# Performance work log

Measured on AMD Instinct MI355X. Metric: run time of the kernel, lower is better.

The kernel has to match this reference:

```python
import jax, jax.numpy as jnp
import numpy as np

NHEAD = 12
EPS = 1e-5


def layernorm_nobias(x, gamma):
    mu = jnp.mean(x, axis=-1, keepdims=True)
    var = jnp.var(x, axis=-1, keepdims=True)
    return (x - mu) * jax.lax.rsqrt(var + EPS) * gamma


def setup_inputs() -> dict:
    key = jax.random.key(0)
    ks = jax.random.split(key, 10)
    b, l, d = 4, 2048, 768
    s = d ** -0.5
    return {
        "x": jax.random.normal(ks[0], (b, l, d), jnp.float32),
        "Wq": jax.random.normal(ks[1], (d, d), jnp.float32) * s,
        "Wk": jax.random.normal(ks[2], (d, d), jnp.float32) * s,
        "bk": jax.random.normal(ks[3], (d,), jnp.float32) * 0.02,
        "Wv": jax.random.normal(ks[4], (d, d), jnp.float32) * s,
        "bv": jax.random.normal(ks[5], (d,), jnp.float32) * 0.02,
        "gq": jnp.ones((d,), jnp.float32),
        "gk": jnp.ones((d,), jnp.float32),
        "Wo": jax.random.normal(ks[6], (d, d), jnp.float32) * s,
        "bo": jnp.zeros((d,), jnp.float32),
    }


def reference(x, Wq, Wk, bk, Wv, bv, gq, gk, Wo, bo):
    b, l, d = x.shape
    n = NHEAD
    hd = d // n
    scale = hd ** -0.5
    # projections (torch Linear: x @ W.T + b), QK-norm over full dmodel
    q = layernorm_nobias(x @ Wq.T, gq)
    k = layernorm_nobias(x @ Wk.T + bk, gk)
    v = x @ Wv.T + bv
    # split heads: b l (n hd) -> b n l hd
    q = q.reshape(b, l, n, hd).transpose(0, 2, 1, 3)
    k = k.reshape(b, l, n, hd).transpose(0, 2, 1, 3)
    v = v.reshape(b, l, n, hd).transpose(0, 2, 1, 3)
    # scores [b, n, l_q, l_k]; NOTE: softmax over the QUERY axis (dim=-2)
    scores = jnp.einsum('bnqd,bnkd->bnqk', q, k) * scale
    attn = jax.nn.softmax(scores, axis=-2)
    o = jnp.einsum('bnqk,bnkd->bnqd', attn, v)
    o = o.transpose(0, 2, 1, 3).reshape(b, l, d)
    return o @ Wo.T + bo + x
```

## Files before the change

### kernel.cpp

```cpp
#include <hip/hip_runtime.h>
#include <cstddef>
#include <cstdint>


typedef unsigned short u16;
typedef short  bf16x8 __attribute__((ext_vector_type(8)));
typedef float  f32x4  __attribute__((ext_vector_type(4)));
typedef unsigned short u16x8 __attribute__((ext_vector_type(8)));
typedef unsigned short u16x4 __attribute__((ext_vector_type(4)));

#define B_   4
#define L_   2048
#define D_   768
#define NH_  12
#define HD_  64
#define M_   (B_*L_)
#define SC2  (0.125f * 1.44269504088896f)

__device__ __forceinline__ float ex2(float x) { return __builtin_amdgcn_exp2f(x); }

__device__ __forceinline__ u16 f2bf(float f) {
    union { float f; unsigned u; } v; v.f = f;
    unsigned r = v.u + 0x7FFFu + ((v.u >> 16) & 1u);
    return (u16)(r >> 16);
}
__device__ __forceinline__ float bf2f(u16 b) {
    union { unsigned u; float f; } v; v.u = ((unsigned)b) << 16;
    return v.f;
}
__device__ __forceinline__ unsigned fbits(float f) {
    union { float f; unsigned u; } v; v.f = f; return v.u;
}
__device__ __forceinline__ unsigned packbf(float lo, float hi) {
    return __builtin_amdgcn_perm(fbits(hi), fbits(lo), 0x07060302u);
}

__device__ __forceinline__ void gld16(const void* g, void* l) {
    __builtin_amdgcn_global_load_lds(
        (const __attribute__((address_space(1))) unsigned*)g,
        (__attribute__((address_space(3))) unsigned*)l, 16, 0, 0);
}

__global__ __launch_bounds__(256) void cvt_all(
    const float* __restrict__ X,
    const float* __restrict__ W0, const float* __restrict__ W1,
    const float* __restrict__ W2, const float* __restrict__ W3,
    u16* __restrict__ Yx,
    u16* __restrict__ Y0, u16* __restrict__ Y1,
    u16* __restrict__ Y2, u16* __restrict__ Y3)
{
    const int nX8 = (M_ * D_) / 8;
    const int nW8 = (D_ * D_) / 8;
    int i = blockIdx.x * 256 + threadIdx.x;
    if (i >= nX8 + 4 * nW8) return;
    const float* S; u16* Dst; int off;
    if (i < nX8) { S = X; Dst = Yx; off = i; }
    else {
        int j = i - nX8;
        int w = j / nW8; off = j - w * nW8;
        S   = (w == 0) ? W0 : (w == 1) ? W1 : (w == 2) ? W2 : W3;
        Dst = (w == 0) ? Y0 : (w == 1) ? Y1 : (w == 2) ? Y2 : Y3;
    }
    const float4* xp = (const float4*)S + (size_t)off * 2;
    float4 a = xp[0], b = xp[1];
    u16x8 o;
    o[0] = f2bf(a.x); o[1] = f2bf(a.y); o[2] = f2bf(a.z); o[3] = f2bf(a.w);
    o[4] = f2bf(b.x); o[5] = f2bf(b.y); o[6] = f2bf(b.z); o[7] = f2bf(b.w);
    *((u16x8*)Dst + off) = o;
}

__global__ __launch_bounds__(256, 4) void gemm_qkv(
    const u16* __restrict__ A,
    const u16* __restrict__ W0, const u16* __restrict__ W1,
    const u16* __restrict__ W2,
    const float* __restrict__ bk, const float* __restrict__ bv,
    u16* __restrict__ q_o, u16* __restrict__ k_o, u16* __restrict__ v_o)
{
    __shared__ __align__(16) u16 lds[16384];
    __shared__ float bs[128];
    const int tid  = threadIdx.x;
    const int lane = tid & 63, w = tid >> 6;
    const int s    = lane & 15, quad = lane >> 4;
    const int bid  = blockIdx.x;
    const int xcd  = bid & 7, j0 = bid >> 3;
    const int bm   = (xcd * 8 + j0 / 18) * 128;
    const int sub  = j0 % 18;
    const int seg  = sub / 6;
    const int bn   = (sub % 6) * 128;
    const u16* W = (seg == 0) ? W0 : ((seg == 1) ? W1 : W2);
    u16* OUT = (seg == 0) ? q_o : ((seg == 1) ? k_o : v_o);
    const int mh = (w >> 1) * 64, nh = (w & 1) * 64;
    const int wb = tid & ~63;
    const int cq = quad ^ ((s >> 1) & 3);

    if (tid < 128)
        bs[tid] = (seg == 1) ? bk[bn + tid] : ((seg == 2) ? bv[bn + tid] : 0.0f);

    f32x4 acc[4][4];
    #pragma unroll
    for (int j = 0; j < 4; ++j)
        #pragma unroll
        for (int i = 0; i < 4; ++i) acc[j][i] = (f32x4){0.f, 0.f, 0.f, 0.f};

    {
        int c = tid, r = c >> 2, cs = (c & 3) ^ ((r >> 1) & 3);
        gld16(A + (size_t)(bm + r) * D_ + cs * 8, lds + (size_t)wb * 8);
        gld16(W + (size_t)(bn + r) * D_ + cs * 8, lds + 8192 + (size_t)wb * 8);
        c = tid + 256; r = c >> 2; cs = (c & 3) ^ ((r >> 1) & 3);
        gld16(A + (size_t)(bm + r) * D_ + cs * 8, lds + (size_t)(wb + 256) * 8);
        gld16(W + (size_t)(bn + r) * D_ + cs * 8, lds + 8192 + (size_t)(wb + 256) * 8);
    }
    __syncthreads();

    for (int t = 0; t < 24; ++t) {
        const u16* Ab = lds + (t & 1) * 4096;
        const u16* Bb = lds + 8192 + (t & 1) * 4096;
        if (t < 23) {
            const int k0 = (t + 1) * 32;
            u16* Ad = lds + ((t + 1) & 1) * 4096;
            u16* Bd = lds + 8192 + ((t + 1) & 1) * 4096;
            int c = tid, r = c >> 2, cs = (c & 3) ^ ((r >> 1) & 3);
            gld16(A + (size_t)(bm + r) * D_ + k0 + cs * 8, Ad + (size_t)wb * 8);
            gld16(W + (size_t)(bn + r) * D_ + k0 + cs * 8, Bd + (size_t)wb * 8);
            c = tid + 256; r = c >> 2; cs = (c & 3) ^ ((r >> 1) & 3);
            gld16(A + (size_t)(bm + r) * D_ + k0 + cs * 8, Ad + (size_t)(wb + 256) * 8);
            gld16(W + (size_t)(bn + r) * D_ + k0 + cs * 8, Bd + (size_t)(wb + 256) * 8);
        }
        bf16x8 af[4], bf[4];
        #pragma unroll
        for (int i = 0; i < 4; ++i)
            af[i] = *(const bf16x8*)(Ab + (mh + i * 16 + s) * 32 + cq * 8);
        #pragma unroll
        for (int j = 0; j < 4; ++j)
            bf[j] = *(const bf16x8*)(Bb + (nh + j * 16 + s) * 32 + cq * 8);
        #pragma unroll
        for (int j = 0; j < 4; ++j)
            #pragma unroll
            for (int i = 0; i < 4; ++i)
                acc[j][i] = __builtin_amdgcn_mfma_f32_16x16x32_bf16(
                    bf[j], af[i], acc[j][i], 0, 0, 0);
        __syncthreads();
    }
    u16* Ct = lds;
    #pragma unroll
    for (int j = 0; j < 4; ++j) {
        const int n0 = nh + j * 16 + quad * 4;
        const f32x4 b4 = *(const f32x4*)(bs + n0);
        const int cn = n0 >> 3, off = n0 & 7;
        #pragma unroll
        for (int i = 0; i < 4; ++i) {
            const int m = mh + i * 16 + s;
            u16x4 ov;
            #pragma unroll
            for (int r = 0; r < 4; ++r) ov[r] = f2bf(acc[j][i][r] + b4[r]);
            *(u16x4*)(Ct + m * 128 + ((cn ^ (m & 15)) * 8) + off) = ov;
        }
    }
    __syncthreads();
    {
        const int m = tid >> 1, half = tid & 1;
        u16* dst = OUT + (size_t)(bm + m) * D_ + bn + half * 64;
        #pragma unroll
        for (int cc = 0; cc < 8; ++cc) {
            const int cn = half * 8 + cc;
            u16x8 v = *(const u16x8*)(Ct + m * 128 + ((cn ^ (m & 15)) * 8));
            *(u16x8*)(dst + cc * 8) = v;
        }
    }
}

__global__ __launch_bounds__(256, 3) void gemm_final(
    const u16* __restrict__ A, const u16* __restrict__ W,
    const float* __restrict__ bias, const float* __restrict__ resid,
    float* __restrict__ outf)
{
    __shared__ __align__(16) u16 lds[16384];
    const int tid  = threadIdx.x;
    const int lane = tid & 63, w = tid >> 6;
    const int s    = lane & 15, quad = lane >> 4;
    const int bid  = blockIdx.x;
    const int xcd  = bid & 7, j0 = bid >> 3;
    const int bm   = (xcd * 8 + j0 / 6) * 128;
    const int bn   = (j0 % 6) * 128;
    const int mh   = (w >> 1) * 64, nh = (w & 1) * 64;
    const int wb   = tid & ~63;
    const int cq   = quad ^ ((s >> 1) & 3);
    f32x4 acc[4][4];
    #pragma unroll
    for (int j = 0; j < 4; ++j)
        #pragma unroll
        for (int i = 0; i < 4; ++i) acc[j][i] = (f32x4){0.f, 0.f, 0.f, 0.f};

    {
        int c = tid, r = c >> 2, cs = (c & 3) ^ ((r >> 1) & 3);
        gld16(A + (size_t)(bm + r) * D_ + cs * 8, lds + (size_t)wb * 8);
        gld16(W + (size_t)(bn + r) * D_ + cs * 8, lds + 8192 + (size_t)wb * 8);
        c = tid + 256; r = c >> 2; cs = (c & 3) ^ ((r >> 1) & 3);
        gld16(A + (size_t)(bm + r) * D_ + cs * 8, lds + (size_t)(wb + 256) * 8);
        gld16(W + (size_t)(bn + r) * D_ + cs * 8, lds + 8192 + (size_t)(wb + 256) * 8);
    }
    __syncthreads();

    for (int t = 0; t < 24; ++t) {
        const u16* Ab = lds + (t & 1) * 4096;
        const u16* Bb = lds + 8192 + (t & 1) * 4096;
        if (t < 23) {
            const int k0 = (t + 1) * 32;
            u16* Ad = lds + ((t + 1) & 1) * 4096;
            u16* Bd = lds + 8192 + ((t + 1) & 1) * 4096;
            int c = tid, r = c >> 2, cs = (c & 3) ^ ((r >> 1) & 3);
            gld16(A + (size_t)(bm + r) * D_ + k0 + cs * 8, Ad + (size_t)wb * 8);
            gld16(W + (size_t)(bn + r) * D_ + k0 + cs * 8, Bd + (size_t)wb * 8);
            c = tid + 256; r = c >> 2; cs = (c & 3) ^ ((r >> 1) & 3);
            gld16(A + (size_t)(bm + r) * D_ + k0 + cs * 8, Ad + (size_t)(wb + 256) * 8);
            gld16(W + (size_t)(bn + r) * D_ + k0 + cs * 8, Bd + (size_t)(wb + 256) * 8);
        }
        bf16x8 af[4], bf[4];
        #pragma unroll
        for (int i = 0; i < 4; ++i)
            af[i] = *(const bf16x8*)(Ab + (mh + i * 16 + s) * 32 + cq * 8);
        #pragma unroll
        for (int j = 0; j < 4; ++j)
            bf[j] = *(const bf16x8*)(Bb + (nh + j * 16 + s) * 32 + cq * 8);
        #pragma unroll
        for (int j = 0; j < 4; ++j)
            #pragma unroll
            for (int i = 0; i < 4; ++i)
                acc[j][i] = __builtin_amdgcn_mfma_f32_16x16x32_bf16(
                    bf[j], af[i], acc[j][i], 0, 0, 0);
        __syncthreads();
    }
    #pragma unroll
    for (int j = 0; j < 4; ++j) {
        const int n0 = nh + j * 16 + quad * 4;
        const float4 b4 = *(const float4*)(bias + bn + n0);
        #pragma unroll
        for (int i = 0; i < 4; ++i) {
            const int m = mh + i * 16 + s;
            const size_t base = (size_t)(bm + m) * D_ + bn + n0;
            const float4 rs = *(const float4*)(resid + base);
            float4 o;
            o.x = acc[j][i][0] + b4.x + rs.x;
            o.y = acc[j][i][1] + b4.y + rs.y;
            o.z = acc[j][i][2] + b4.z + rs.z;
            o.w = acc[j][i][3] + b4.w + rs.w;
            *(float4*)(outf + base) = o;
        }
    }
}

__global__ __launch_bounds__(256) void ln2_bf16(
    const u16* __restrict__ Q, const u16* __restrict__ K,
    const float* __restrict__ gq, const float* __restrict__ gk,
    u16* __restrict__ Yq, u16* __restrict__ Yk)
{
    const int which = blockIdx.y;
    const int rowi  = threadIdx.x >> 5;
    const int l32   = threadIdx.x & 31;
    const int row   = blockIdx.x * 8 + rowi;
    const u16* x = (which ? K : Q) + (size_t)row * D_ + l32 * 24;
    const float* gamma = (which ? gk : gq) + l32 * 24;
    u16* Y = (which ? Yk : Yq) + (size_t)row * D_ + l32 * 24;
    const float scale = which ? 1.0f : (float)SC2;

    u16x8 vv[3];
    float f[24];
    float lsum = 0.f, lsq = 0.f;
    #pragma unroll
    for (int e = 0; e < 3; ++e) {
        vv[e] = *(const u16x8*)(x + e * 8);
        #pragma unroll
        for (int k = 0; k < 8; ++k) {
            float t = bf2f(vv[e][k]);
            f[e * 8 + k] = t; lsum += t; lsq += t * t;
        }
    }
    #pragma unroll
    for (int off = 16; off > 0; off >>= 1) {
        lsum += __shfl_xor(lsum, off);
        lsq  += __shfl_xor(lsq,  off);
    }
    const float mu  = lsum * (1.0f / D_);
    const float var = lsq * (1.0f / D_) - mu * mu;
    const float inv = rsqrtf(var + 1e-5f) * scale;
    #pragma unroll
    for (int e = 0; e < 3; ++e) {
        const float4 ga = *(const float4*)(gamma + e * 8);
        const float4 gb = *(const float4*)(gamma + e * 8 + 4);
        u16x8 o;
        o[0] = f2bf((f[e*8+0] - mu) * inv * ga.x);
        o[1] = f2bf((f[e*8+1] - mu) * inv * ga.y);
        o[2] = f2bf((f[e*8+2] - mu) * inv * ga.z);
        o[3] = f2bf((f[e*8+3] - mu) * inv * ga.w);
        o[4] = f2bf((f[e*8+4] - mu) * inv * gb.x);
        o[5] = f2bf((f[e*8+5] - mu) * inv * gb.y);
        o[6] = f2bf((f[e*8+6] - mu) * inv * gb.z);
        o[7] = f2bf((f[e*8+7] - mu) * inv * gb.w);
        *(u16x8*)(Y + e * 8) = o;
    }
}

__global__ __launch_bounds__(256, 3) void attn_stats(
    const u16* __restrict__ Qb, const u16* __restrict__ Kb,
    const u16* __restrict__ Vb, u16* __restrict__ Vt)
{
    __shared__ __align__(16) u16 Ks[128 * 64];
    __shared__ __align__(16) u16 Qs[2][128 * 64];
    __shared__ float lbuf[4][64];
    __shared__ float rls[128];
    const int tid  = threadIdx.x;
    const int lane = tid & 63, w = tid >> 6;
    const int s    = lane & 15, quad = lane >> 4;
    const int s7   = s & 7;
    const int bid  = blockIdx.x;
    const int xcd  = bid & 7, j0 = bid >> 3;
    const int bh   = xcd * 6 + j0 / 16;
    const int kbase = (j0 % 16) * 128;
    const int b    = bh / NH_, h = bh % NH_;
    const u16* Qg = Qb + (size_t)b * L_ * D_ + h * HD_;
    const u16* Kg = Kb + (size_t)b * L_ * D_ + h * HD_;
    const int mh = (w >> 1) * 64;
    const int nh = (w & 1) * 64;
    const int wb = tid & ~63;

    #pragma unroll
    for (int c0 = 0; c0 < 1024; c0 += 256) {
        int c = c0 + tid, r = c >> 3, cc = (c & 7) ^ (r & 7);
        gld16(Kg + (size_t)(kbase + r) * D_ + cc * 8, Ks + (size_t)(c0 + wb) * 8);
        gld16(Qg + (size_t)r * D_ + cc * 8, Qs[0] + (size_t)(c0 + wb) * 8);
    }
    __syncthreads();
    bf16x8 kf[2][4];
    #pragma unroll
    for (int kk = 0; kk < 2; ++kk)
        #pragma unroll
        for (int i = 0; i < 4; ++i)
            kf[kk][i] = *(const bf16x8*)(Ks + (mh + i * 16 + s) * 64 +
                                         ((kk * 4 + quad) ^ s7) * 8);
    float lacc[4][4];
    #pragma unroll
    for (int i = 0; i < 4; ++i)
        #pragma unroll
        for (int r = 0; r < 4; ++r) lacc[i][r] = 0.f;

    for (int t = 0; t < 16; ++t) {
        if (t < 15) {
            const int qn = (t + 1) * 128;
            u16* Qd = Qs[(t + 1) & 1];
            #pragma unroll
            for (int c0 = 0; c0 < 1024; c0 += 256) {
                int c = c0 + tid, r = c >> 3, cc = (c & 7) ^ (r & 7);
                gld16(Qg + (size_t)(qn + r) * D_ + cc * 8, Qd + (size_t)(c0 + wb) * 8);
            }
        }
        const u16* Qt = Qs[t & 1];
        f32x4 acc[4][4];
        #pragma unroll
        for (int i = 0; i < 4; ++i)
            #pragma unroll
            for (int j = 0; j < 4; ++j) acc[i][j] = (f32x4){0.f, 0.f, 0.f, 0.f};
        #pragma unroll
        for (int kk = 0; kk < 2; ++kk) {
            bf16x8 bf[4];
            #pragma unroll
            for (int j = 0; j < 4; ++j)
                bf[j] = *(const bf16x8*)(Qt + (nh + j * 16 + s) * 64 +
                                         ((kk * 4 + quad) ^ s7) * 8);
            __builtin_amdgcn_s_setprio(1);
            #pragma unroll
            for (int i = 0; i < 4; ++i)
                #pragma unroll
                for (int j = 0; j < 4; ++j)
                    acc[i][j] = __builtin_amdgcn_mfma_f32_16x16x32_bf16(
                        kf[kk][i], bf[j], acc[i][j], 0, 0, 0);
            __builtin_amdgcn_s_setprio(0);
        }
        #pragma unroll
        for (int i = 0; i < 4; ++i)
            #pragma unroll
            for (int r = 0; r < 4; ++r) {
                float l0 = ex2(acc[i][0][r]) + ex2(acc[i][1][r]);
                float l1 = ex2(acc[i][2][r]) + ex2(acc[i][3][r]);
                lacc[i][r] += l0 + l1;
            }
        __syncthreads();
    }
    #pragma unroll
    for (int i = 0; i < 4; ++i)
        #pragma unroll
        for (int r = 0; r < 4; ++r) {
            float v = lacc[i][r];
            #pragma unroll
            for (int d2 = 1; d2 < 16; d2 <<= 1) v += __shfl_xor(v, d2);
            lacc[i][r] = v;
        }
    if (s == 0) {
        #pragma unroll
        for (int i = 0; i < 4; ++i)
            #pragma unroll
            for (int r = 0; r < 4; ++r)
                lbuf[w][i * 16 + quad * 4 + r] = lacc[i][r];
    }
    __syncthreads();
    if (tid < 128) {
        int kh = tid >> 6, kl = tid & 63;
        float l = lbuf[kh * 2][kl] + lbuf[kh * 2 + 1][kl];
        rls[tid] = 1.0f / l;
    }
    __syncthreads();

    u16 (*Ts)[72] = (u16 (*)[72])(&Qs[0][0]);
    for (int half = 0; half < 2; ++half) {
        const int l0g = kbase + half * 64;
        for (int c = tid; c < 512; c += 256) {
            int r = c >> 3, cc = c & 7;
            u16x8 val = *(const u16x8*)(Vb + (size_t)(b * L_ + l0g + r) * D_ +
                                        h * HD_ + cc * 8);
            const float rl = rls[half * 64 + r];
            #pragma unroll
            for (int e = 0; e < 8; ++e) val[e] = f2bf(bf2f(val[e]) * rl);
            *(u16x8*)(&Ts[r][cc * 8]) = val;
        }
        __syncthreads();
        const int d = tid >> 2, lc = (tid & 3) * 16;
        u16 tmp[16];
        #pragma unroll
        for (int e = 0; e < 16; ++e) tmp[e] = Ts[lc + e][d];
        u16* dst = Vt + ((size_t)bh * HD_ + d) * L_ + l0g + (lc & 32) +
                   ((lc >> 4) & 1) * 4;
        #pragma unroll
        for (int qd = 0; qd < 4; ++qd) {
            u16x4 o;
            #pragma unroll
            for (int e = 0; e < 4; ++e) o[e] = tmp[qd * 4 + e];
            *(u16x4*)(dst + qd * 8) = o;
        }
        __syncthreads();
    }
}

__global__ __launch_bounds__(256, 3) void attn_out(
    const u16* __restrict__ Qb, const u16* __restrict__ Kb,
    const u16* __restrict__ Vt, u16* __restrict__ Ob)
{
    __shared__ __align__(16) u16 Ks[3][64 * 64];
    __shared__ __align__(16) u16 Vts[3][64 * 64];
    const int tid  = threadIdx.x;
    const int lane = tid & 63, w = tid >> 6;
    const int s    = lane & 15, quad = lane >> 4;
    const int s7   = s & 7;
    const int bid  = blockIdx.x;
    const int xcd  = bid & 7, j0 = bid >> 3;
    const int bh   = xcd * 6 + j0 / 16;
    const int qbase = (j0 % 16) * 128;
    const int b    = bh / NH_, h = bh % NH_;
    const int qw   = w * 32;
    const u16* Qg = Qb + (size_t)b * L_ * D_ + h * HD_;
    const u16* Kg = Kb + (size_t)b * L_ * D_ + h * HD_;
    const u16* Vg = Vt + (size_t)bh * HD_ * L_;
    const int wb = tid & ~63;

    bf16x8 qf[2][2];
    #pragma unroll
    for (int kk = 0; kk < 2; ++kk)
        #pragma unroll
        for (int j = 0; j < 2; ++j)
            qf[kk][j] = *(const bf16x8*)(
                Qg + (size_t)(qbase + qw + j * 16 + s) * D_ + (kk * 4 + quad) * 8);

    {
        int c = tid, r = c >> 3, cc = (c & 7) ^ (r & 7);
        int c2 = tid + 256, r2 = c2 >> 3, cc2 = (c2 & 7) ^ (r2 & 7);
        gld16(Kg + (size_t)r * D_ + cc * 8,          Ks[0] + (size_t)wb * 8);
        gld16(Kg + (size_t)r2 * D_ + cc2 * 8,        Ks[0] + (size_t)(wb + 256) * 8);
        gld16(Kg + (size_t)(64 + r) * D_ + cc * 8,   Ks[1] + (size_t)wb * 8);
        gld16(Kg + (size_t)(64 + r2) * D_ + cc2 * 8, Ks[1] + (size_t)(wb + 256) * 8);
        gld16(Vg + (size_t)r * L_ + cc * 8,          Vts[0] + (size_t)wb * 8);
        gld16(Vg + (size_t)r2 * L_ + cc2 * 8,        Vts[0] + (size_t)(wb + 256) * 8);
        gld16(Vg + (size_t)r * L_ + 64 + cc * 8,     Vts[1] + (size_t)wb * 8);
        gld16(Vg + (size_t)r2 * L_ + 64 + cc2 * 8,   Vts[1] + (size_t)(wb + 256) * 8);
    }
    asm volatile("s_waitcnt vmcnt(2)" ::: "memory");
    __builtin_amdgcn_s_barrier();

    f32x4 acc_o[4][2];
    #pragma unroll
    for (int i = 0; i < 4; ++i)
        #pragma unroll
        for (int j = 0; j < 2; ++j) acc_o[i][j] = (f32x4){0.f, 0.f, 0.f, 0.f};

    f32x4 acc_s0[4][2], acc_s1[4][2];
    #pragma unroll
    for (int i = 0; i < 4; ++i)
        #pragma unroll
        for (int j = 0; j < 2; ++j) acc_s0[i][j] = (f32x4){0.f, 0.f, 0.f, 0.f};
    #pragma unroll
    for (int kk = 0; kk < 2; ++kk) {
        bf16x8 kfr[4];
        #pragma unroll
        for (int i = 0; i < 4; ++i)
            kfr[i] = *(const bf16x8*)(Ks[0] + (i * 16 + s) * 64 +
                                      ((kk * 4 + quad) ^ s7) * 8);
        #pragma unroll
        for (int i = 0; i < 4; ++i)
            #pragma unroll
            for (int j = 0; j < 2; ++j)
                acc_s0[i][j] = __builtin_amdgcn_mfma_f32_16x16x32_bf16(
                    kfr[i], qf[kk][j], acc_s0[i][j], 0, 0, 0);
    }

#define ATTN_TILE(ACCC, ACCN, TT, DO_PF, DO_S, WMODE)                          \
    do {                                                                       \
        const int t_ = (TT);                                                   \
        if (DO_PF) {                                                           \
            const int pi_ = (t_ + 2) % 3;                                      \
            const int kn_ = (t_ + 2) * 64;                                     \
            u16* Kd_ = Ks[pi_]; u16* Vd_ = Vts[pi_];                           \
            int c_ = tid, r_ = c_ >> 3, cc_ = (c_ & 7) ^ (r_ & 7);             \
            int c2_ = tid + 256, r2_ = c2_ >> 3, cc2_ = (c2_ & 7) ^ (r2_ & 7); \
            gld16(Kg + (size_t)(kn_ + r_) * D_ + cc_ * 8,                      \
                  Kd_ + (size_t)wb * 8);                                       \
            gld16(Kg + (size_t)(kn_ + r2_) * D_ + cc2_ * 8,                    \
                  Kd_ + (size_t)(wb + 256) * 8);                               \
            gld16(Vg + (size_t)r_ * L_ + kn_ + cc_ * 8,                        \
                  Vd_ + (size_t)wb * 8);                                       \
            gld16(Vg + (size_t)r2_ * L_ + kn_ + cc2_ * 8,                      \
                  Vd_ + (size_t)(wb + 256) * 8);                               \
        }                                                                      \
                 \
        unsigned pk_[4][2][2];                                                 \
        _Pragma("unroll")                                                      \
        for (int i = 0; i < 4; ++i)                                            \
            _Pragma("unroll")                                                  \
            for (int j = 0; j < 2; ++j) {                                      \
                float p0_ = ex2(ACCC[i][j][0]), p1_ = ex2(ACCC[i][j][1]);      \
                float p2_ = ex2(ACCC[i][j][2]), p3_ = ex2(ACCC[i][j][3]);      \
                pk_[i][j][0] = packbf(p0_, p1_);                               \
                pk_[i][j][1] = packbf(p2_, p3_);                               \
            }                                                                  \
        if (DO_S) {                                                            \
            const u16* Kt_ = Ks[(t_ + 1) % 3];                                 \
            _Pragma("unroll")                                                  \
            for (int i = 0; i < 4; ++i)                                        \
                _Pragma("unroll")                                              \
                for (int j = 0; j < 2; ++j)                                    \
                    ACCN[i][j] = (f32x4){0.f, 0.f, 0.f, 0.f};                  \
            _Pragma("unroll")                                                  \
            for (int kk = 0; kk < 2; ++kk) {                                   \
                bf16x8 kfr_[4];                                                \
                _Pragma("unroll")                                              \
                for (int i = 0; i < 4; ++i)                                    \
                    kfr_[i] = *(const bf16x8*)(Kt_ + (i * 16 + s) * 64 +       \
                                               ((kk * 4 + quad) ^ s7) * 8);    \
                _Pragma("unroll")                                              \
                for (int i = 0; i < 4; ++i)                                    \
                    _Pragma("unroll")                                          \
                    for (int j = 0; j < 2; ++j)                                \
                        ACCN[i][j] = __builtin_amdgcn_mfma_f32_16x16x32_bf16(  \
                            kfr_[i], qf[kk][j], ACCN[i][j], 0, 0, 0);          \
            }                                                                  \
        }                                                                      \
                                                                   \
        {                                                                      \
            const u16* Vtt_ = Vts[t_ % 3];                                     \
            _Pragma("unroll")                                                  \
            for (int kk = 0; kk < 2; ++kk) {                                   \
                bf16x8 av_[4];                                                 \
                _Pragma("unroll")                                              \
                for (int i = 0; i < 4; ++i)                                    \
                    av_[i] = *(const bf16x8*)(Vtt_ + (i * 16 + s) * 64 +       \
                                              ((kk * 4 + quad) ^ s7) * 8);     \
                __builtin_amdgcn_s_setprio(1);                                 \
                _Pragma("unroll")                                              \
                for (int j = 0; j < 2; ++j) {                                  \
                    union { unsigned u[4]; bf16x8 v; } bu_;                    \
                    bu_.u[0] = pk_[2 * kk][j][0];                              \
                    bu_.u[1] = pk_[2 * kk][j][1];                              \
                    bu_.u[2] = pk_[2 * kk + 1][j][0];                          \
                    bu_.u[3] = pk_[2 * kk + 1][j][1];                          \
                    _Pragma("unroll")                                          \
                    for (int i = 0; i < 4; ++i)                                \
                        acc_o[i][j] = __builtin_amdgcn_mfma_f32_16x16x32_bf16( \
                            av_[i], bu_.v, acc_o[i][j], 0, 0, 0);              \
                }                                                              \
                __builtin_amdgcn_s_setprio(0);                                 \
            }                                                                  \
        }                                                                      \
        if (WMODE == 2) {                                                      \
            asm volatile("s_waitcnt vmcnt(2)" ::: "memory");                   \
            __builtin_amdgcn_s_barrier();                                      \
        } else if (WMODE == 0) {                                               \
            asm volatile("s_waitcnt vmcnt(0)" ::: "memory");                   \
            __builtin_amdgcn_s_barrier();                                      \
        }                                                                      \
    } while (0)

    for (int t = 0; t < 30; t += 2) {
        ATTN_TILE(acc_s0, acc_s1, t,     1, 1, 2);
        ATTN_TILE(acc_s1, acc_s0, t + 1, 1, 1, 2);
    }
    ATTN_TILE(acc_s0, acc_s1, 30, 0, 1, 0);
    ATTN_TILE(acc_s1, acc_s0, 31, 0, 0, -1);
#undef ATTN_TILE

    __syncthreads();
    u16* Ep = (u16*)Ks;
    #pragma unroll
    for (int i = 0; i < 4; ++i) {
        const int dchunk = i * 2 + (quad >> 1), doff = (quad & 1) * 4;
        #pragma unroll
        for (int j = 0; j < 2; ++j) {
            const int q = qw + j * 16 + s;
            u16x4 ov;
            #pragma unroll
            for (int r = 0; r < 4; ++r) ov[r] = f2bf(acc_o[i][j][r]);
            *(u16x4*)(Ep + q * 64 + (dchunk ^ s7) * 8 + doff) = ov;
        }
    }
    __syncthreads();
    {
        const int q = tid >> 1, half = tid & 1, q7 = q & 7;
        u16* dst = Ob + (size_t)(b * L_ + qbase + q) * D_ + h * HD_ + half * 32;
        #pragma unroll
        for (int c = 0; c < 4; ++c) {
            const int cn = half * 4 + c;
            u16x8 v = *(const u16x8*)(Ep + q * 64 + ((cn ^ q7) * 8));
            *(u16x8*)(dst + c * 8) = v;
        }
    }
}

extern "C" void kernel_launch(void* const* d_in, const int* in_sizes, int n_in,
                              void* d_out, int out_size, void* d_ws, size_t ws_size,
                              hipStream_t stream)
{
    const float* x  = (const float*)d_in[0];
    const float* Wq = (const float*)d_in[1];
    const float* Wk = (const float*)d_in[2];
    const float* bk = (const float*)d_in[3];
    const float* Wv = (const float*)d_in[4];
    const float* bv = (const float*)d_in[5];
    const float* gq = (const float*)d_in[6];
    const float* gk = (const float*)d_in[7];
    const float* Wo = (const float*)d_in[8];
    const float* bo = (const float*)d_in[9];
    float* out = (float*)d_out;

    char* p = (char*)d_ws;
    u16* xb   = (u16*)p;  p += (size_t)M_ * D_ * 2;
    u16* qpre = (u16*)p;  p += (size_t)M_ * D_ * 2;
    u16* kpre = (u16*)p;  p += (size_t)M_ * D_ * 2;
    u16* vb   = (u16*)p;  p += (size_t)M_ * D_ * 2;
    u16* qb   = (u16*)p;  p += (size_t)M_ * D_ * 2;
    u16* kb   = (u16*)p;  p += (size_t)M_ * D_ * 2;
    u16* wqb  = (u16*)p;  p += (size_t)D_ * D_ * 2;
    u16* wkb  = (u16*)p;  p += (size_t)D_ * D_ * 2;
    u16* wvb  = (u16*)p;  p += (size_t)D_ * D_ * 2;
    u16* wob  = (u16*)p;  p += (size_t)D_ * D_ * 2;
    u16* ob = qpre;
    u16* vt = kpre;

    const int nTot8 = (M_ * D_ + 4 * D_ * D_) / 8;
    cvt_all<<<(nTot8 + 255) / 256, 256, 0, stream>>>(
        x, Wq, Wk, Wv, Wo, xb, wqb, wkb, wvb, wob);

    gemm_qkv<<<1152, 256, 0, stream>>>(
        xb, wqb, wkb, wvb, bk, bv, qpre, kpre, vb);

    ln2_bf16<<<dim3(M_ / 8, 2), 256, 0, stream>>>(qpre, kpre, gq, gk, qb, kb);

    attn_stats<<<768, 256, 0, stream>>>(qb, kb, vb, vt);
    attn_out<<<768, 256, 0, stream>>>(qb, kb, vt, ob);

    gemm_final<<<384, 256, 0, stream>>>(ob, wob, bo, x, out);
}
```

Measured before the change: 266.9 us.

## Triple-buffer LDS in projection GEMMs with two-stage-ahead async prefetch

Both projection GEMMs (QKV and output) go from double to triple LDS buffering and prefetch tiles two K-steps ahead. The full __syncthreads is replaced by a partial vmcnt wait plus a raw barrier, so the loads for the next-next tile stay in flight while the current tile computes. This hides more global-load latency, but the larger LDS footprint lowers launch bounds occupancy for gemm_qkv from 4 to 3 blocks.

```diff
diff --git a/kernel.cpp b/kernel.cpp
--- a/kernel.cpp
+++ b/kernel.cpp
@@ -69,14 +69,14 @@
     *((u16x8*)Dst + off) = o;
 }
 
-__global__ __launch_bounds__(256, 4) void gemm_qkv(
+__global__ __launch_bounds__(256, 3) void gemm_qkv(
     const u16* __restrict__ A,
     const u16* __restrict__ W0, const u16* __restrict__ W1,
     const u16* __restrict__ W2,
     const float* __restrict__ bk, const float* __restrict__ bv,
     u16* __restrict__ q_o, u16* __restrict__ k_o, u16* __restrict__ v_o)
 {
-    __shared__ __align__(16) u16 lds[16384];
+    __shared__ __align__(16) u16 lds[24576];
     __shared__ float bs[128];
     const int tid  = threadIdx.x;
     const int lane = tid & 63, w = tid >> 6;
@@ -104,27 +104,34 @@
 
     {
         int c = tid, r = c >> 2, cs = (c & 3) ^ ((r >> 1) & 3);
-        gld16(A + (size_t)(bm + r) * D_ + cs * 8, lds + (size_t)wb * 8);
-        gld16(W + (size_t)(bn + r) * D_ + cs * 8, lds + 8192 + (size_t)wb * 8);
-        c = tid + 256; r = c >> 2; cs = (c & 3) ^ ((r >> 1) & 3);
-        gld16(A + (size_t)(bm + r) * D_ + cs * 8, lds + (size_t)(wb + 256) * 8);
-        gld16(W + (size_t)(bn + r) * D_ + cs * 8, lds + 8192 + (size_t)(wb + 256) * 8);
-    }
-    __syncthreads();
+        int c2 = tid + 256, r2 = c2 >> 2, cs2 = (c2 & 3) ^ ((r2 >> 1) & 3);
+        gld16(A + (size_t)(bm + r) * D_ + cs * 8,        lds + (size_t)wb * 8);
+        gld16(W + (size_t)(bn + r) * D_ + cs * 8,        lds + 12288 + (size_t)wb * 8);
+        gld16(A + (size_t)(bm + r2) * D_ + cs2 * 8,      lds + (size_t)(wb + 256) * 8);
+        gld16(W + (size_t)(bn + r2) * D_ + cs2 * 8,      lds + 12288 + (size_t)(wb + 256) * 8);
+        gld16(A + (size_t)(bm + r) * D_ + 32 + cs * 8,   lds + 4096 + (size_t)wb * 8);
+        gld16(W + (size_t)(bn + r) * D_ + 32 + cs * 8,   lds + 16384 + (size_t)wb * 8);
+        gld16(A + (size_t)(bm + r2) * D_ + 32 + cs2 * 8, lds + 4096 + (size_t)(wb + 256) * 8);
+        gld16(W + (size_t)(bn + r2) * D_ + 32 + cs2 * 8, lds + 16384 + (size_t)(wb + 256) * 8);
+    }
+    asm volatile("s_waitcnt vmcnt(4)" ::: "memory");
+    __builtin_amdgcn_s_barrier();
 
     for (int t = 0; t < 24; ++t) {
-        const u16* Ab = lds + (t & 1) * 4096;
-        const u16* Bb = lds + 8192 + (t & 1) * 4096;
-        if (t < 23) {
-            const int k0 = (t + 1) * 32;
-            u16* Ad = lds + ((t + 1) & 1) * 4096;
-            u16* Bd = lds + 8192 + ((t + 1) & 1) * 4096;
+        const int bi = t % 3;
+        const u16* Ab = lds + bi * 4096;
+        const u16* Bb = lds + 12288 + bi * 4096;
+        if (t < 22) {
+            const int pi = (t + 2) % 3;
+            const int k0 = (t + 2) * 32;
+            u16* Ad = lds + pi * 4096;
+            u16* Bd = lds + 12288 + pi * 4096;
             int c = tid, r = c >> 2, cs = (c & 3) ^ ((r >> 1) & 3);
-            gld16(A + (size_t)(bm + r) * D_ + k0 + cs * 8, Ad + (size_t)wb * 8);
-            gld16(W + (size_t)(bn + r) * D_ + k0 + cs * 8, Bd + (size_t)wb * 8);
-            c = tid + 256; r = c >> 2; cs = (c & 3) ^ ((r >> 1) & 3);
-            gld16(A + (size_t)(bm + r) * D_ + k0 + cs * 8, Ad + (size_t)(wb + 256) * 8);
-            gld16(W + (size_t)(bn + r) * D_ + k0 + cs * 8, Bd + (size_t)(wb + 256) * 8);
+            int c2 = tid + 256, r2 = c2 >> 2, cs2 = (c2 & 3) ^ ((r2 >> 1) & 3);
+            gld16(A + (size_t)(bm + r) * D_ + k0 + cs * 8,   Ad + (size_t)wb * 8);
+            gld16(W + (size_t)(bn + r) * D_ + k0 + cs * 8,   Bd + (size_t)wb * 8);
+            gld16(A + (size_t)(bm + r2) * D_ + k0 + cs2 * 8, Ad + (size_t)(wb + 256) * 8);
+            gld16(W + (size_t)(bn + r2) * D_ + k0 + cs2 * 8, Bd + (size_t)(wb + 256) * 8);
         }
         bf16x8 af[4], bf[4];
         #pragma unroll
@@ -139,8 +146,15 @@
             for (int i = 0; i < 4; ++i)
                 acc[j][i] = __builtin_amdgcn_mfma_f32_16x16x32_bf16(
                     bf[j], af[i], acc[j][i], 0, 0, 0);
-        __syncthreads();
-    }
+        if (t < 22) {
+            asm volatile("s_waitcnt vmcnt(4)" ::: "memory");
+            __builtin_amdgcn_s_barrier();
+        } else if (t == 22) {
+            asm volatile("s_waitcnt vmcnt(0)" ::: "memory");
+            __builtin_amdgcn_s_barrier();
+        }
+    }
+    __syncthreads();
     u16* Ct = lds;
     #pragma unroll
     for (int j = 0; j < 4; ++j) {
@@ -174,7 +188,7 @@
     const float* __restrict__ bias, const float* __restrict__ resid,
     float* __restrict__ outf)
 {
-    __shared__ __align__(16) u16 lds[16384];
+    __shared__ __align__(16) u16 lds[24576];
     const int tid  = threadIdx.x;
     const int lane = tid & 63, w = tid >> 6;
     const int s    = lane & 15, quad = lane >> 4;
@@ -193,27 +207,34 @@
 
     {
         int c = tid, r = c >> 2, cs = (c & 3) ^ ((r >> 1) & 3);
-        gld16(A + (size_t)(bm + r) * D_ + cs * 8, lds + (size_t)wb * 8);
-        gld16(W + (size_t)(bn + r) * D_ + cs * 8, lds + 8192 + (size_t)wb * 8);
-        c = tid + 256; r = c >> 2; cs = (c & 3) ^ ((r >> 1) & 3);
-        gld16(A + (size_t)(bm + r) * D_ + cs * 8, lds + (size_t)(wb + 256) * 8);
-        gld16(W + (size_t)(bn + r) * D_ + cs * 8, lds + 8192 + (size_t)(wb + 256) * 8);
-    }
-    __syncthreads();
+        int c2 = tid + 256, r2 = c2 >> 2, cs2 = (c2 & 3) ^ ((r2 >> 1) & 3);
+        gld16(A + (size_t)(bm + r) * D_ + cs * 8,        lds + (size_t)wb * 8);
+        gld16(W + (size_t)(bn + r) * D_ + cs * 8,        lds + 12288 + (size_t)wb * 8);
+        gld16(A + (size_t)(bm + r2) * D_ + cs2 * 8,      lds + (size_t)(wb + 256) * 8);
+        gld16(W + (size_t)(bn + r2) * D_ + cs2 * 8,      lds + 12288 + (size_t)(wb + 256) * 8);
+        gld16(A + (size_t)(bm + r) * D_ + 32 + cs * 8,   lds + 4096 + (size_t)wb * 8);
+        gld16(W + (size_t)(bn + r) * D_ + 32 + cs * 8,   lds + 16384 + (size_t)wb * 8);
+        gld16(A + (size_t)(bm + r2) * D_ + 32 + cs2 * 8, lds + 4096 + (size_t)(wb + 256) * 8);
+        gld16(W + (size_t)(bn + r2) * D_ + 32 + cs2 * 8, lds + 16384 + (size_t)(wb + 256) * 8);
+    }
+    asm volatile("s_waitcnt vmcnt(4)" ::: "memory");
+    __builtin_amdgcn_s_barrier();
 
     for (int t = 0; t < 24; ++t) {
-        const u16* Ab = lds + (t & 1) * 4096;
-        const u16* Bb = lds + 8192 + (t & 1) * 4096;
-        if (t < 23) {
-            const int k0 = (t + 1) * 32;
-            u16* Ad = lds + ((t + 1) & 1) * 4096;
-            u16* Bd = lds + 8192 + ((t + 1) & 1) * 4096;
+        const int bi = t % 3;
+        const u16* Ab = lds + bi * 4096;
+        const u16* Bb = lds + 12288 + bi * 4096;
+        if (t < 22) {
+            const int pi = (t + 2) % 3;
+            const int k0 = (t + 2) * 32;
+            u16* Ad = lds + pi * 4096;
+            u16* Bd = lds + 12288 + pi * 4096;
             int c = tid, r = c >> 2, cs = (c & 3) ^ ((r >> 1) & 3);
-            gld16(A + (size_t)(bm + r) * D_ + k0 + cs * 8, Ad + (size_t)wb * 8);
-            gld16(W + (size_t)(bn + r) * D_ + k0 + cs * 8, Bd + (size_t)wb * 8);
-            c = tid + 256; r = c >> 2; cs = (c & 3) ^ ((r >> 1) & 3);
-            gld16(A + (size_t)(bm + r) * D_ + k0 + cs * 8, Ad + (size_t)(wb + 256) * 8);
-            gld16(W + (size_t)(bn + r) * D_ + k0 + cs * 8, Bd + (size_t)(wb + 256) * 8);
+            int c2 = tid + 256, r2 = c2 >> 2, cs2 = (c2 & 3) ^ ((r2 >> 1) & 3);
+            gld16(A + (size_t)(bm + r) * D_ + k0 + cs * 8,   Ad + (size_t)wb * 8);
+            gld16(W + (size_t)(bn + r) * D_ + k0 + cs * 8,   Bd + (size_t)wb * 8);
+            gld16(A + (size_t)(bm + r2) * D_ + k0 + cs2 * 8, Ad + (size_t)(wb + 256) * 8);
+            gld16(W + (size_t)(bn + r2) * D_ + k0 + cs2 * 8, Bd + (size_t)(wb + 256) * 8);
         }
         bf16x8 af[4], bf[4];
         #pragma unroll
@@ -228,7 +249,13 @@
             for (int i = 0; i < 4; ++i)
                 acc[j][i] = __builtin_amdgcn_mfma_f32_16x16x32_bf16(
                     bf[j], af[i], acc[j][i], 0, 0, 0);
-        __syncthreads();
+        if (t < 22) {
+            asm volatile("s_waitcnt vmcnt(4)" ::: "memory");
+            __builtin_amdgcn_s_barrier();
+        } else if (t == 22) {
+            asm volatile("s_waitcnt vmcnt(0)" ::: "memory");
+            __builtin_amdgcn_s_barrier();
+        }
     }
     #pragma unroll
     for (int j = 0; j < 4; ++j) {
```

Result: no change. 268.5 us (+0.6%).
